# Performance work log

Hardware: AMD Instinct MI355X
Metric: run time of the kernel (lower is better)

The kernel has to match this reference:

```python
import jax, jax.numpy as jnp
import numpy as np

B, N, E = 32, 128, 8192        # graphs, nodes/graph, edges total
IN, ED, H = 64, 32, 128        # node feat, edge feat, hidden
K1, K2, K3 = 64, 32, 16        # ceil(0.5*N) cascade from TopKPooling(ratio=0.5)
EPS = 1e-5


def setup_inputs():
    key = jax.random.key(0)
    ks = jax.random.split(key, 20)
    def rn(i, shape, s=1.0):
        return jax.random.normal(ks[i], shape, dtype=jnp.float32) * s
    x = rn(0, (B * N, IN))
    edge_attr = rn(1, (E, ED))
    epg = E // B  # edges per graph (intra-graph only)
    src = jax.random.randint(ks[2], (B, epg), 0, N)
    dst = jax.random.randint(ks[3], (B, epg), 0, N)
    off = (jnp.arange(B) * N)[:, None]
    edge_index = jnp.stack([(src + off).reshape(-1), (dst + off).reshape(-1)]).astype(jnp.int32)
    batch = jnp.repeat(jnp.arange(B), N).astype(jnp.int32)
    p = {}
    p['nn1_w'] = rn(4, (ED, IN * H), 0.05); p['nn1_b'] = jnp.zeros((IN * H,), jnp.float32)
    p['root1'] = rn(5, (IN, H), 0.1);       p['bias1'] = jnp.zeros((H,), jnp.float32)
    p['nn2_w'] = rn(6, (ED, H * H), 0.05);  p['nn2_b'] = jnp.zeros((H * H,), jnp.float32)
    p['root2'] = rn(7, (H, H), 0.1);        p['bias2'] = jnp.zeros((H,), jnp.float32)
    p['nn3_w'] = rn(8, (ED, H * H), 0.05);  p['nn3_b'] = jnp.zeros((H * H,), jnp.float32)
    p['root3'] = rn(9, (H, H), 0.1);        p['bias3'] = jnp.zeros((H,), jnp.float32)
    for k in ('1', '2', '3'):
        p['gamma' + k] = jnp.ones((H,), jnp.float32)
        p['beta' + k] = jnp.zeros((H,), jnp.float32)
    p['pw1'] = rn(10, (H,), 0.1); p['pw2'] = rn(11, (H,), 0.1); p['pw3'] = rn(12, (H,), 0.1)
    p['lin1_w'] = rn(13, (H, H // 2), 0.1); p['lin1_b'] = jnp.zeros((H // 2,), jnp.float32)
    p['lin2_w'] = rn(14, (H // 2, 1), 0.1); p['lin2_b'] = jnp.zeros((1,), jnp.float32)
    return dict(x=x, edge_index=edge_index, edge_attr=edge_attr, batch=batch, **p)


def _nnconv(x, src, dst, emask, eattr, nn_w, nn_b, root, bias, cin, cout, n_nodes):
    # per-edge weight matrix from edge MLP: [E, cin, cout]
    w = (eattr @ nn_w + nn_b).reshape(-1, cin, cout)
    msg = jnp.einsum('ei,eio->eo', x[src], w) * emask[:, None]  # per-edge matvec
    agg = jnp.zeros((n_nodes, cout), x.dtype).at[dst].add(msg)  # scatter-add aggr
    return agg + x @ root + bias


def _bn(x, gamma, beta):
    mu = x.mean(0)
    var = x.var(0)
    return gamma * (x - mu) * jax.lax.rsqrt(var + EPS) + beta


def _topk_pool(x, src, dst, emask, pw, nb, npg, k):
    # PyG TopKPooling: score = tanh((x.p)/||p||); keep top ceil(ratio*n) per graph
    score = jnp.tanh((x @ pw) / jnp.linalg.norm(pw))            # [nb*npg]
    _, idx = jax.lax.top_k(score.reshape(nb, npg), k)           # [nb, k]
    perm = (idx + (jnp.arange(nb) * npg)[:, None]).reshape(-1)  # global node ids
    x_new = x[perm] * score[perm][:, None]
    mapping = jnp.full((nb * npg,), -1, jnp.int32).at[perm].set(
        jnp.arange(nb * k, dtype=jnp.int32))
    ns, nd = mapping[src], mapping[dst]
    valid = (ns >= 0) & (nd >= 0) & emask   # filter_adj via mask, static shapes
    return x_new, jnp.where(valid, ns, 0), jnp.where(valid, nd, 0), valid


def _forward(x, edge_attr, nn1_w, nn1_b, root1, bias1, gamma1, beta1, pw1,
             nn2_w, nn2_b, root2, bias2, gamma2, beta2, pw2,
             nn3_w, nn3_b, root3, bias3, gamma3, beta3, pw3,
             lin1_w, lin1_b, lin2_w, lin2_b, edge_index):
    src0, dst0 = edge_index[0], edge_index[1]
    m0 = jnp.ones((E,), bool)
    h = _nnconv(x, src0, dst0, m0, edge_attr, nn1_w, nn1_b, root1, bias1, IN, H, B * N)
    h = jax.nn.relu(_bn(h, gamma1, beta1))
    h, s1, d1, m1 = _topk_pool(h, src0, dst0, m0, pw1, B, N, K1)
    h = _nnconv(h, s1, d1, m1, edge_attr, nn2_w, nn2_b, root2, bias2, H, H, B * K1)
    h = jax.nn.relu(_bn(h, gamma2, beta2))
    h, s2, d2, m2 = _topk_pool(h, s1, d1, m1, pw2, B, K1, K2)
    h = _nnconv(h, s2, d2, m2, edge_attr, nn3_w, nn3_b, root3, bias3, H, H, B * K2)
    h = jax.nn.relu(_bn(h, gamma3, beta3))
    h, _, _, _ = _topk_pool(h, s2, d2, m2, pw3, B, K2, K3)
    g = h.reshape(B, K3, H).mean(axis=1)          # global_mean_pool (equal-size graphs)
    g = jax.nn.relu(g @ lin1_w + lin1_b)          # dropout is identity in eval mode
    return jax.nn.sigmoid(g @ lin2_w + lin2_b)    # [B, 1]


def reference(x, edge_index, edge_attr, batch,
              nn1_w, nn1_b, root1, bias1, nn2_w, nn2_b, root2, bias2,
              nn3_w, nn3_b, root3, bias3, gamma1, beta1, gamma2, beta2,
              gamma3, beta3, pw1, pw2, pw3, lin1_w, lin1_b, lin2_w, lin2_b):
    return _forward(x, edge_attr, nn1_w, nn1_b, root1, bias1, gamma1, beta1, pw1,
                    nn2_w, nn2_b, root2, bias2, gamma2, beta2, pw2,
                    nn3_w, nn3_b, root3, bias3, gamma3, beta3, pw3,
                    lin1_w, lin1_b, lin2_w, lin2_b, edge_index)
```

## Files before the change

### kernel.cpp

```cpp
#include <hip/hip_runtime.h>

#define E_TOT 8192
#define NB    32
#define H     128
#define EPG   256
#define NDT   34
#define YD    33
#define YCOLS (YD * H)

#define KH1   2176
#define TROW1 (2 * KH1)
#define KSPLIT1 12

typedef __attribute__((ext_vector_type(8))) short bf16x8;
typedef __attribute__((ext_vector_type(4))) float f32x4;

__device__ __forceinline__ unsigned short bf16_rne(float f) {
    unsigned int u = __float_as_uint(f);
    unsigned int r = (u + 0x7FFFu + ((u >> 16) & 1u)) >> 16;
    return (unsigned short)r;
}
__device__ __forceinline__ float bf16_to_f32(unsigned short h) {
    return __uint_as_float(((unsigned int)h) << 16);
}

__device__ __forceinline__ void gload_lds16(const void* g, void* l) {
    __builtin_amdgcn_global_load_lds(
        (const __attribute__((address_space(1))) unsigned int*)g,
        (__attribute__((address_space(3))) unsigned int*)l, 16, 0, 0);
}

union PrepSMem {
    struct { unsigned short HI[128][72]; unsigned short LO[128][72]; } b1;
    struct { unsigned short HI[128][40]; unsigned short LO[128][40]; } bt;
    struct { float xL[128][64]; float eaL[256][32]; short srcL[256];
             short lists[16][256]; int cnt[16]; } t1;
};

__global__ __launch_bounds__(256)
void prep_all(const float* __restrict__ x, const float* __restrict__ ea,
              const int* __restrict__ esrc, const int* __restrict__ edst,
              const float* __restrict__ nn1w, const float* __restrict__ nn1b,
              const float* __restrict__ root1,
              const float* __restrict__ nn2w, const float* __restrict__ nn2b,
              const float* __restrict__ root2,
              const float* __restrict__ nn3w, const float* __restrict__ nn3b,
              const float* __restrict__ root3,
              unsigned short* __restrict__ Bt1, unsigned short* __restrict__ Bt2,
              unsigned short* __restrict__ Bt3, unsigned short* __restrict__ T1,
              float* __restrict__ stats)
{
    __shared__ PrepSMem sm;
    const int b   = blockIdx.x;
    const int tid = threadIdx.x;

    if (b < 34) {
        if (b == 0)
            for (int i = tid; i < 768; i += 256) stats[i] = 0.f;
        const int d = b;
        const float* __restrict__ W =
            (d < 32) ? (nn1w + (size_t)d * 8192) : ((d == 32) ? nn1b : root1);
        for (int idx = tid; idx < 64 * 128; idx += 256) {
            const int ii = idx >> 7, o = idx & 127;
            const float v = W[ii * 128 + o];
            const unsigned short h = bf16_rne(v);
            sm.b1.HI[o][ii] = h;
            sm.b1.LO[o][ii] = bf16_rne(v - bf16_to_f32(h));
        }
        __syncthreads();
        const int o = tid & 127, half = tid >> 7;
        const uint4* s4 = (const uint4*)(half ? &sm.b1.LO[o][0] : &sm.b1.HI[o][0]);
        uint4* d4 = (uint4*)(Bt1 + (size_t)o * TROW1 + (half ? KH1 : 0) + d * 64);
        #pragma unroll
        for (int q = 0; q < 8; ++q) d4[q] = s4[q];
    } else if (b < 306) {
        const int unit  = b - 34;
        const int stage = unit / 136;
        const int u2    = unit - stage * 136;
        const int d  = u2 >> 2;
        const int i0 = (u2 & 3) * 32;
        const float* __restrict__ W = (stage == 0)
            ? ((d < 32) ? (nn2w + (size_t)d * 16384) : ((d == 32) ? nn2b : root2))
            : ((d < 32) ? (nn3w + (size_t)d * 16384) : ((d == 32) ? nn3b : root3));
        unsigned short* __restrict__ Bt = (stage == 0) ? Bt2 : Bt3;

        for (int idx = tid; idx < 32 * 128; idx += 256) {
            const int ii = idx >> 7, o = idx & 127;
            const float v = W[(size_t)(i0 + ii) * 128 + o];
            const unsigned short h = bf16_rne(v);
            sm.bt.HI[o][ii] = h;
            sm.bt.LO[o][ii] = bf16_rne(v - bf16_to_f32(h));
        }
        __syncthreads();
        const int o = tid & 127, half = tid >> 7;
        unsigned short* dst = Bt + (size_t)(d * 128 + o) * 384;
        const uint4* hs = (const uint4*)&sm.bt.HI[o][0];
        const uint4* ls = (const uint4*)&sm.bt.LO[o][0];
        if (half == 0) {
            uint4* p = (uint4*)(dst + i0);
            p[0] = hs[0]; p[1] = hs[1]; p[2] = hs[2]; p[3] = hs[3];
            uint4* q = (uint4*)(dst + 256 + i0);
            q[0] = ls[0]; q[1] = ls[1]; q[2] = ls[2]; q[3] = ls[3];
        } else {
            uint4* p = (uint4*)(dst + 128 + i0);
            p[0] = hs[0]; p[1] = hs[1]; p[2] = hs[2]; p[3] = hs[3];
        }
    } else {
        const int u    = b - 306;
        const int g    = u >> 3;
        const int base = (u & 7) * 16;
        const int wv   = tid >> 6;
        const int ln   = tid & 63;

        if (tid < 16) sm.t1.cnt[tid] = 0;
        for (int idx = tid; idx < 128 * 64; idx += 256)
            sm.t1.xL[idx >> 6][idx & 63] = x[(size_t)g * 8192 + idx];
        for (int idx = tid; idx < 256 * 32; idx += 256)
            sm.t1.eaL[idx >> 5][idx & 31] = ea[(size_t)g * 8192 + idx];
        __syncthreads();

        {
            const int e = tid;
            sm.t1.srcL[e] = (short)(esrc[g * EPG + e] - g * 128);
            const int r = (edst[g * EPG + e] - g * 128) - base;
            if (r >= 0 && r < 16) {
                const int pos = atomicAdd(&sm.t1.cnt[r], 1);
                sm.t1.lists[r][pos] = (short)e;
            }
        }
        __syncthreads();

        #pragma unroll
        for (int j = 0; j < 4; ++j) {
            const int r = wv * 4 + j;
            const int uu = base + r;
            float acc[33];
            #pragma unroll
            for (int d = 0; d < 33; ++d) acc[d] = 0.f;

            const int n = sm.t1.cnt[r];
            for (int t = 0; t < n; ++t) {
                const int e = sm.t1.lists[r][t];
                const float xv = sm.t1.xL[sm.t1.srcL[e]][ln];
                #pragma unroll
                for (int d = 0; d < 32; ++d) acc[d] += sm.t1.eaL[e][d] * xv;
                acc[32] += xv;
            }

            unsigned short* row = T1 + (size_t)(g * 128 + uu) * TROW1;
            #pragma unroll
            for (int d = 0; d < 33; ++d) {
                const unsigned short hb = bf16_rne(acc[d]);
                row[d * 64 + ln] = hb;
                row[KH1 + d * 64 + ln] = bf16_rne(acc[d] - bf16_to_f32(hb));
            }
            const float xv = sm.t1.xL[uu][ln];
            const unsigned short hb = bf16_rne(xv);
            row[2112 + ln] = hb;
            row[KH1 + 2112 + ln] = bf16_rne(xv - bf16_to_f32(hb));
        }
    }
}

__global__ __launch_bounds__(256)
void hgemm1(const unsigned short* __restrict__ A,
            const unsigned short* __restrict__ Bt,
            const float* __restrict__ bias,
            float* __restrict__ hpart)
{
    __shared__ unsigned short Alds[128 * 32];
    __shared__ unsigned short Blds[128 * 32];

    const int lane = threadIdx.x & 63;
    const int w    = threadIdx.x >> 6;
    const int wm = w >> 1, wn = w & 1;
    const int v0 = blockIdx.x * 128;
    const int c  = blockIdx.y;

    f32x4 acc[4][4];
    #pragma unroll
    for (int i = 0; i < 4; ++i)
        #pragma unroll
        for (int j = 0; j < 4; ++j)
            acc[i][j] = (f32x4)(0.0f);

    const int arow = lane >> 2;
    const int acol = (lane & 3) * 8;
    const int koff = (lane >> 4) * 8;
    const int mrow = lane & 15;

    for (int t = c * 17; t < c * 17 + 17; ++t) {
        const int s  = t / 68;
        const int ko = (t - s * 68) * 32;
        const int aoff = (s == 2 ? KH1 : 0) + ko;
        const int boff = (s == 1 ? KH1 : 0) + ko;

        __syncthreads();
        #pragma unroll
        for (int tt = 0; tt < 2; ++tt) {
            const int cc = w * 2 + tt;
            const int r = cc * 16 + arow;
            gload_lds16(A  + (size_t)(v0 + r) * TROW1 + aoff + acol, &Alds[cc * 512]);
            gload_lds16(Bt + (size_t)r * TROW1 + boff + acol, &Blds[cc * 512]);
        }
        __syncthreads();

        bf16x8 a[4], b[4];
        #pragma unroll
        for (int f = 0; f < 4; ++f) {
            a[f] = *(const bf16x8*)&Alds[(wm * 64 + f * 16 + mrow) * 32 + koff];
            b[f] = *(const bf16x8*)&Blds[(wn * 64 + f * 16 + mrow) * 32 + koff];
        }
        #pragma unroll
        for (int fm = 0; fm < 4; ++fm)
            #pragma unroll
            for (int fn = 0; fn < 4; ++fn)
                acc[fm][fn] = __builtin_amdgcn_mfma_f32_16x16x32_bf16(
                    a[fm], b[fn], acc[fm][fn], 0, 0, 0);
    }

    float* out = hpart + (size_t)c * (4096 * 128);
    const int crow = (lane >> 4) * 4;
    const int ccol = lane & 15;
    #pragma unroll
    for (int fm = 0; fm < 4; ++fm) {
        const int gr = v0 + wm * 64 + fm * 16 + crow;
        #pragma unroll
        for (int fn = 0; fn < 4; ++fn) {
            const int col = wn * 64 + fn * 16 + ccol;
            const float bv = (c == 0) ? bias[col] : 0.f;
            #pragma unroll
            for (int r = 0; r < 4; ++r)
                out[(size_t)(gr + r) * H + col] = acc[fm][fn][r] + bv;
        }
    }
}

__global__ __launch_bounds__(256)
void bn_reduce1(const float* __restrict__ hpart, float* __restrict__ h1,
                float* __restrict__ gsum, float* __restrict__ gsumsq)
{
    const int tid   = threadIdx.x;
    const int col   = tid & 127;
    const int rhalf = tid >> 7;
    float s = 0.f, sq = 0.f;
    for (int r = blockIdx.x * 2 + rhalf; r < 4096; r += gridDim.x * 2) {
        float v = 0.f;
        #pragma unroll
        for (int c = 0; c < KSPLIT1; ++c)
            v += hpart[(size_t)c * (4096 * 128) + (size_t)r * H + col];
        h1[(size_t)r * H + col] = v;
        s += v; sq += v * v;
    }
    __shared__ float sh[256];
    sh[tid] = s;  __syncthreads();
    if (rhalf == 0) s += sh[tid + 128];
    __syncthreads();
    sh[tid] = sq; __syncthreads();
    if (rhalf == 0) {
        sq += sh[tid + 128];
        atomicAdd(&gsum[col], s);
        atomicAdd(&gsumsq[col], sq);
    }
}

template<int K3>
__global__ __launch_bounds__(256)
void ygemm_mfma(const unsigned short* __restrict__ A,
                const unsigned short* __restrict__ Bt,
                float* __restrict__ Y,
                const float* __restrict__ bias,
                float* __restrict__ h)
{
    __shared__ unsigned short Alds[128 * 32];
    __shared__ unsigned short Blds[128 * 32];

    const int lane = threadIdx.x & 63;
    const int w    = threadIdx.x >> 6;
    const int wm = w >> 1, wn = w & 1;
    const int v0 = blockIdx.x * 128;
    const int n0 = blockIdx.y * 128;

    f32x4 acc[4][4];
    #pragma unroll
    for (int i = 0; i < 4; ++i)
        #pragma unroll
        for (int j = 0; j < 4; ++j)
            acc[i][j] = (f32x4)(0.0f);

    const int arow = lane >> 2;
    const int acol = (lane & 3) * 8;
    const int koff = (lane >> 4) * 8;
    const int mrow = lane & 15;

    for (int k0 = 0; k0 < K3; k0 += 32) {
        __syncthreads();
        #pragma unroll
        for (int t = 0; t < 2; ++t) {
            const int c = w * 2 + t;
            const int r = c * 16 + arow;
            gload_lds16(A  + (size_t)(v0 + r) * K3 + k0 + acol, &Alds[c * 512]);
            gload_lds16(Bt + (size_t)(n0 + r) * K3 + k0 + acol, &Blds[c * 512]);
        }
        __syncthreads();

        bf16x8 a[4], b[4];
        #pragma unroll
        for (int f = 0; f < 4; ++f) {
            a[f] = *(const bf16x8*)&Alds[(wm * 64 + f * 16 + mrow) * 32 + koff];
            b[f] = *(const bf16x8*)&Blds[(wn * 64 + f * 16 + mrow) * 32 + koff];
        }
        #pragma unroll
        for (int fm = 0; fm < 4; ++fm)
            #pragma unroll
            for (int fn = 0; fn < 4; ++fn)
                acc[fm][fn] = __builtin_amdgcn_mfma_f32_16x16x32_bf16(
                    a[fm], b[fn], acc[fm][fn], 0, 0, 0);
    }

    const int crow = (lane >> 4) * 4;
    const int ccol = lane & 15;
    const bool is_root = (blockIdx.y == YD);
    #pragma unroll
    for (int fm = 0; fm < 4; ++fm) {
        const int gr = v0 + wm * 64 + fm * 16 + crow;
        #pragma unroll
        for (int fn = 0; fn < 4; ++fn) {
            const int col = wn * 64 + fn * 16 + ccol;
            if (is_root) {
                const float bv = bias[col];
                #pragma unroll
                for (int r = 0; r < 4; ++r)
                    h[(size_t)(gr + r) * H + col] = acc[fm][fn][r] + bv;
            } else {
                const size_t gc = (size_t)blockIdx.y * H + col;
                #pragma unroll
                for (int r = 0; r < 4; ++r)
                    Y[(size_t)(gr + r) * YCOLS + gc] = acc[fm][fn][r];
            }
        }
    }
}

__global__ __launch_bounds__(256)
void contract_edges(const float* __restrict__ Y,
                    const float* __restrict__ ea,
                    const int*   __restrict__ esrc,
                    const int*   __restrict__ edst,
                    float*       __restrict__ agg)
{
    const int grp = threadIdx.x >> 5;
    const int l5  = threadIdx.x & 31;
    const int e   = blockIdx.x * 8 + grp;
    const int s   = esrc[e];
    if (s < 0) return;

    const float* yb  = Y + (size_t)s * YCOLS + l5 * 4;
    const float* ear = ea + (size_t)e * 32;

    float4 acc = *reinterpret_cast<const float4*>(yb + 32 * H);
    #pragma unroll 8
    for (int dd = 0; dd < 32; ++dd) {
        const float c = ear[dd];
        const float4 y = *reinterpret_cast<const float4*>(yb + dd * H);
        acc.x += c * y.x; acc.y += c * y.y; acc.z += c * y.z; acc.w += c * y.w;
    }
    float* out = agg + (size_t)edst[e] * H + l5 * 4;
    atomicAdd(out + 0, acc.x);
    atomicAdd(out + 1, acc.y);
    atomicAdd(out + 2, acc.z);
    atomicAdd(out + 3, acc.w);
}

__global__ __launch_bounds__(256)
void bn_stats(const float* __restrict__ h, int n,
              float* __restrict__ gsum, float* __restrict__ gsumsq)
{
    const int tid   = threadIdx.x;
    const int col   = tid & 127;
    const int rhalf = tid >> 7;
    float s = 0.f, sq = 0.f;
    for (int r = blockIdx.x * 2 + rhalf; r < n; r += gridDim.x * 2) {
        float v = h[(size_t)r * H + col];
        s += v; sq += v * v;
    }
    __shared__ float sh[256];
    sh[tid] = s;  __syncthreads();
    if (rhalf == 0) s += sh[tid + 128];
    __syncthreads();
    sh[tid] = sq; __syncthreads();
    if (rhalf == 0) {
        sq += sh[tid + 128];
        atomicAdd(&gsum[col], s);
        atomicAdd(&gsumsq[col], sq);
    }
}

__global__ __launch_bounds__(256)
void fused_pool(const float* __restrict__ h,
                const float* __restrict__ gsum, const float* __restrict__ gsumsq,
                float n_f,
                const float* __restrict__ gamma, const float* __restrict__ beta,
                const float* __restrict__ pw,
                int npg, int k,
                const int* __restrict__ esrc_in, const int* __restrict__ edst_in,
                int* __restrict__ esrc_out, int* __restrict__ edst_out,
                unsigned short* __restrict__ Aout)
{
    const int g   = blockIdx.x;
    const int tid = threadIdx.x;
    const int wv  = tid >> 6;
    const int ln  = tid & 63;

    __shared__ float muL[128], rsL[128], gmL[128], btL[128], pwL[128];
    __shared__ float scoreL[128], red[128];
    __shared__ int   mapL[128];
    __shared__ float sinv;

    if (tid < 128) {
        const float mu  = gsum[tid] / n_f;
        const float var = gsumsq[tid] / n_f - mu * mu;
        muL[tid] = mu;
        rsL[tid] = rsqrtf(var + 1e-5f);
        gmL[tid] = gamma[tid];
        btL[tid] = beta[tid];
        const float p = pw[tid];
        pwL[tid] = p;
        red[tid] = p * p;
    }
    __syncthreads();
    for (int off = 64; off > 0; off >>= 1) {
        if (tid < off) red[tid] += red[tid + off];
        __syncthreads();
    }
    if (tid == 0) sinv = rsqrtf(red[0]);
    __syncthreads();

    for (int r = wv; r < npg; r += 4) {
        const float* hr = h + (size_t)(g * npg + r) * H;
        float p = 0.f;
        #pragma unroll
        for (int half = 0; half < 2; ++half) {
            const int c = ln + half * 64;
            const float y = fmaxf(gmL[c] * (hr[c] - muL[c]) * rsL[c] + btL[c], 0.f);
            p += y * pwL[c];
        }
        #pragma unroll
        for (int off = 32; off > 0; off >>= 1)
            p += __shfl_down(p, off, 64);
        if (ln == 0) scoreL[r] = tanhf(p * sinv);
    }
    __syncthreads();

    if (tid < npg) {
        const float si = scoreL[tid];
        int cnt = 0;
        for (int j = 0; j < npg; ++j) {
            const float sj = scoreL[j];
            cnt += (sj > si) || (sj == si && j < tid);
        }
        mapL[tid] = (cnt < k) ? cnt : -1;
    }
    __syncthreads();

    for (int r = wv; r < npg; r += 4) {
        const int nr = mapL[r];
        if (nr < 0) continue;
        const float sc = scoreL[r];
        const float* hr = h + (size_t)(g * npg + r) * H;
        unsigned short* arow = Aout + (size_t)(g * k + nr) * 384;
        #pragma unroll
        for (int half = 0; half < 2; ++half) {
            const int c = ln + half * 64;
            const float y = fmaxf(gmL[c] * (hr[c] - muL[c]) * rsL[c] + btL[c], 0.f) * sc;
            const unsigned short hb = bf16_rne(y);
            const unsigned short lb = bf16_rne(y - bf16_to_f32(hb));
            arow[c] = hb; arow[128 + c] = hb; arow[256 + c] = lb;
        }
    }

    {
        const int e = g * EPG + tid;
        const int s = esrc_in[e];
        int ns = -1, nd = -1;
        if (s >= 0) {
            const int ms = mapL[s - g * npg];
            const int md = mapL[edst_in[e] - g * npg];
            if (ms >= 0 && md >= 0) { ns = g * k + ms; nd = g * k + md; }
        }
        esrc_out[e] = ns; edst_out[e] = nd;
    }
}

__global__ __launch_bounds__(256)
void fused_pool_final(const float* __restrict__ h,
                      const float* __restrict__ gsum, const float* __restrict__ gsumsq,
                      float n_f,
                      const float* __restrict__ gamma, const float* __restrict__ beta,
                      const float* __restrict__ pw,
                      const float* __restrict__ lin1_w, const float* __restrict__ lin1_b,
                      const float* __restrict__ lin2_w, const float* __restrict__ lin2_b,
                      float* __restrict__ out)
{
    const int g   = blockIdx.x;
    const int tid = threadIdx.x;
    const int wv  = tid >> 6;
    const int ln  = tid & 63;
    const int npg = 32, k = 16;

    __shared__ float muL[128], rsL[128], gmL[128], btL[128], pwL[128];
    __shared__ float scoreL[32], red[128], gmean[128], h1c[64];
    __shared__ int   mapL[32];
    __shared__ float sinv;

    if (tid < 128) {
        const float mu  = gsum[tid] / n_f;
        const float var = gsumsq[tid] / n_f - mu * mu;
        muL[tid] = mu;
        rsL[tid] = rsqrtf(var + 1e-5f);
        gmL[tid] = gamma[tid];
        btL[tid] = beta[tid];
        const float p = pw[tid];
        pwL[tid] = p;
        red[tid] = p * p;
    }
    __syncthreads();
    for (int off = 64; off > 0; off >>= 1) {
        if (tid < off) red[tid] += red[tid + off];
        __syncthreads();
    }
    if (tid == 0) sinv = rsqrtf(red[0]);
    __syncthreads();

    for (int r = wv; r < npg; r += 4) {
        const float* hr = h + (size_t)(g * npg + r) * H;
        float p = 0.f;
        #pragma unroll
        for (int half = 0; half < 2; ++half) {
            const int c = ln + half * 64;
            const float y = fmaxf(gmL[c] * (hr[c] - muL[c]) * rsL[c] + btL[c], 0.f);
            p += y * pwL[c];
        }
        #pragma unroll
        for (int off = 32; off > 0; off >>= 1)
            p += __shfl_down(p, off, 64);
        if (ln == 0) scoreL[r] = tanhf(p * sinv);
    }
    __syncthreads();

    if (tid < npg) {
        const float si = scoreL[tid];
        int cnt = 0;
        for (int j = 0; j < npg; ++j) {
            const float sj = scoreL[j];
            cnt += (sj > si) || (sj == si && j < tid);
        }
        mapL[tid] = (cnt < k) ? cnt : -1;
    }
    __syncthreads();

    if (tid < 128) {
        float acc = 0.f;
        for (int r = 0; r < npg; ++r) {
            if (mapL[r] < 0) continue;
            const float hv = h[(size_t)(g * npg + r) * H + tid];
            const float y  = fmaxf(gmL[tid] * (hv - muL[tid]) * rsL[tid] + btL[tid], 0.f);
            acc += y * scoreL[r];
        }
        gmean[tid] = acc * (1.0f / 16.0f);
    }
    __syncthreads();

    if (tid < 64) {
        float acc = lin1_b[tid];
        for (int o = 0; o < 128; ++o) acc += gmean[o] * lin1_w[o * 64 + tid];
        h1c[tid] = fmaxf(acc, 0.f);
    }
    __syncthreads();
    if (tid == 0) {
        float z = lin2_b[0];
        for (int j = 0; j < 64; ++j) z += h1c[j] * lin2_w[j];
        out[g] = 1.0f / (1.0f + expf(-z));
    }
}

extern "C" void kernel_launch(void* const* d_in, const int* in_sizes, int n_in,
                              void* d_out, int out_size, void* d_ws, size_t ws_size,
                              hipStream_t stream)
{
    const float* x        = (const float*)d_in[0];
    const int*   ei       = (const int*)  d_in[1];
    const float* eattr    = (const float*)d_in[2];
    const float* nn1_w    = (const float*)d_in[4];
    const float* nn1_b    = (const float*)d_in[5];
    const float* root1    = (const float*)d_in[6];
    const float* bias1    = (const float*)d_in[7];
    const float* nn2_w    = (const float*)d_in[8];
    const float* nn2_b    = (const float*)d_in[9];
    const float* root2    = (const float*)d_in[10];
    const float* bias2    = (const float*)d_in[11];
    const float* nn3_w    = (const float*)d_in[12];
    const float* nn3_b    = (const float*)d_in[13];
    const float* root3    = (const float*)d_in[14];
    const float* bias3    = (const float*)d_in[15];
    const float* gamma1   = (const float*)d_in[16];
    const float* beta1    = (const float*)d_in[17];
    const float* gamma2   = (const float*)d_in[18];
    const float* beta2    = (const float*)d_in[19];
    const float* gamma3   = (const float*)d_in[20];
    const float* beta3    = (const float*)d_in[21];
    const float* pw1      = (const float*)d_in[22];
    const float* pw2      = (const float*)d_in[23];
    const float* pw3      = (const float*)d_in[24];
    const float* lin1_w   = (const float*)d_in[25];
    const float* lin1_b   = (const float*)d_in[26];
    const float* lin2_w   = (const float*)d_in[27];
    const float* lin2_b   = (const float*)d_in[28];

    const int* ei_src = ei;
    const int* ei_dst = ei + E_TOT;

    char* wp = (char*)d_ws;
    auto alloc = [&](size_t bytes) { char* p = wp; wp += (bytes + 255) & ~(size_t)255; return p; };
    float* h1   = (float*)alloc(4096 * 128 * 4);
    float* h2   = (float*)alloc(2048 * 128 * 4);
    float* h3   = (float*)alloc(1024 * 128 * 4);
    int*   src1 = (int*)alloc(E_TOT * 4);
    int*   dst1 = (int*)alloc(E_TOT * 4);
    int*   src2 = (int*)alloc(E_TOT * 4);
    int*   dst2 = (int*)alloc(E_TOT * 4);
    float* stats = (float*)alloc(6 * 128 * 4);
    unsigned short* A2   = (unsigned short*)alloc((size_t)2048 * 384 * 2);
    unsigned short* A3   = (unsigned short*)alloc((size_t)1024 * 384 * 2);
    unsigned short* Bt1n = (unsigned short*)alloc((size_t)128 * TROW1 * 2);
    unsigned short* Bt2  = (unsigned short*)alloc((size_t)4352 * 384 * 2);
    unsigned short* Bt3  = (unsigned short*)alloc((size_t)4352 * 384 * 2);
    unsigned short* T1   = (unsigned short*)alloc((size_t)4096 * TROW1 * 2);
    float* hpart = (float*)alloc((size_t)KSPLIT1 * 4096 * 128 * 4);
    float* Ybuf = (float*)alloc((size_t)2048 * YCOLS * 4);

    prep_all<<<562, 256, 0, stream>>>(x, eattr, ei_src, ei_dst,
                                      nn1_w, nn1_b, root1,
                                      nn2_w, nn2_b, root2,
                                      nn3_w, nn3_b, root3,
                                      Bt1n, Bt2, Bt3, T1, stats);

    hgemm1<<<dim3(32, KSPLIT1), 256, 0, stream>>>(T1, Bt1n, bias1, hpart);
    bn_reduce1<<<256, 256, 0, stream>>>(hpart, h1, stats, stats + 128);
    fused_pool<<<NB, 256, 0, stream>>>(h1, stats, stats + 128, 4096.0f,
                                       gamma1, beta1, pw1, 128, 64,
                                       ei_src, ei_dst, src1, dst1, A2);

    ygemm_mfma<384><<<dim3(16, NDT), 256, 0, stream>>>(A2, Bt2, Ybuf, bias2, h2);
    contract_edges<<<E_TOT / 8, 256, 0, stream>>>(Ybuf, eattr, src1, dst1, h2);
    bn_stats<<<64, 256, 0, stream>>>(h2, 2048, stats + 256, stats + 384);
    fused_pool<<<NB, 256, 0, stream>>>(h2, stats + 256, stats + 384, 2048.0f,
                                       gamma2, beta2, pw2, 64, 32,
                                       src1, dst1, src2, dst2, A3);

    ygemm_mfma<384><<<dim3(8, NDT), 256, 0, stream>>>(A3, Bt3, Ybuf, bias3, h3);
    contract_edges<<<E_TOT / 8, 256, 0, stream>>>(Ybuf, eattr, src2, dst2, h3);
    bn_stats<<<64, 256, 0, stream>>>(h3, 1024, stats + 512, stats + 640);
    fused_pool_final<<<NB, 256, 0, stream>>>(h3, stats + 512, stats + 640, 1024.0f,
                                             gamma3, beta3, pw3,
                                             lin1_w, lin1_b, lin2_w, lin2_b,
                                             (float*)d_out);
}
```

Measured before the change: 291.6 us.

## Reformulate NNConv layers 2 and 3 as edge-contracted T-matrix split-K GEMMs

Layers 2 and 3 previously ran a GEMM producing per-node Y matrices for every edge-feature dimension, followed by a per-edge contraction with float atomics into the output. They now follow the layer-1 scheme: a t_build kernel aggregates edge_attr-weighted source features per destination node into a wide bf16 hi/lo T matrix, and a templated split-K GEMM multiplies it by a reorganized weight layout, with partial sums reduced in bn_reduce. This removes the large Ybuf round trip and the scatter atomics. In exchange it adds the T build pass, a wider K dimension, and a 24-way partial buffer to write and reduce.

After: 309.6 us. +6.2%, slower.

```diff
diff --git a/kernel.cpp b/kernel.cpp
--- a/kernel.cpp
+++ b/kernel.cpp
@@ -4,13 +4,11 @@
 #define NB    32
 #define H     128
 #define EPG   256
-#define NDT   34
-#define YD    33
-#define YCOLS (YD * H)
 
 #define KH1   2176
 #define TROW1 (2 * KH1)
-#define KSPLIT1 12
+#define KH2   4352
+#define TROW2 (2 * KH2)
 
 typedef __attribute__((ext_vector_type(8))) short bf16x8;
 typedef __attribute__((ext_vector_type(4))) float f32x4;
@@ -93,18 +91,10 @@
         }
         __syncthreads();
         const int o = tid & 127, half = tid >> 7;
-        unsigned short* dst = Bt + (size_t)(d * 128 + o) * 384;
-        const uint4* hs = (const uint4*)&sm.bt.HI[o][0];
-        const uint4* ls = (const uint4*)&sm.bt.LO[o][0];
-        if (half == 0) {
-            uint4* p = (uint4*)(dst + i0);
-            p[0] = hs[0]; p[1] = hs[1]; p[2] = hs[2]; p[3] = hs[3];
-            uint4* q = (uint4*)(dst + 256 + i0);
-            q[0] = ls[0]; q[1] = ls[1]; q[2] = ls[2]; q[3] = ls[3];
-        } else {
-            uint4* p = (uint4*)(dst + 128 + i0);
-            p[0] = hs[0]; p[1] = hs[1]; p[2] = hs[2]; p[3] = hs[3];
-        }
+        const uint4* s4 = (const uint4*)(half ? &sm.bt.LO[o][0] : &sm.bt.HI[o][0]);
+        uint4* d4 = (uint4*)(Bt + (size_t)o * TROW2 + (half ? KH2 : 0) + d * 128 + i0);
+        #pragma unroll
+        for (int q = 0; q < 4; ++q) d4[q] = s4[q];
     } else {
         const int u    = b - 306;
         const int g    = u >> 3;
@@ -162,12 +152,89 @@
     }
 }
 
+template<int KROWS>
 __global__ __launch_bounds__(256)
-void hgemm1(const unsigned short* __restrict__ A,
-            const unsigned short* __restrict__ Bt,
-            const float* __restrict__ bias,
-            float* __restrict__ hpart)
+void t_build(const float* __restrict__ x2,
+             const float* __restrict__ ea,
+             const int* __restrict__ esrc, const int* __restrict__ edst,
+             unsigned short* __restrict__ T)
 {
+    const int g    = blockIdx.x;
+    const int base = blockIdx.y * 8;
+    const int tid  = threadIdx.x;
+    const int wv   = tid >> 6;
+    const int ln   = tid & 63;
+
+    __shared__ float xL[KROWS][128];
+    __shared__ float eaL[256][32];
+    __shared__ short srcL[256];
+    __shared__ short lists[8][256];
+    __shared__ int   cnt[8];
+
+    if (tid < 8) cnt[tid] = 0;
+    for (int idx = tid; idx < KROWS * 32; idx += 256)
+        ((float4*)&xL[0][0])[idx] = ((const float4*)(x2 + (size_t)g * KROWS * H))[idx];
+    for (int idx = tid; idx < 256 * 8; idx += 256)
+        ((float4*)&eaL[0][0])[idx] = ((const float4*)(ea + (size_t)g * 8192))[idx];
+    __syncthreads();
+
+    {
+        const int e = tid;
+        srcL[e] = (short)(esrc[g * EPG + e] - g * KROWS);
+        const int r = (edst[g * EPG + e] - g * KROWS) - base;
+        if (r >= 0 && r < 8) {
+            const int pos = atomicAdd(&cnt[r], 1);
+            lists[r][pos] = (short)e;
+        }
+    }
+    __syncthreads();
+
+    #pragma unroll
+    for (int j = 0; j < 2; ++j) {
+        const int r = wv * 2 + j;
+        const int u = base + r;
+        unsigned short* row = T + (size_t)(g * KROWS + u) * TROW2;
+        const int n = cnt[r];
+
+        #pragma unroll
+        for (int half = 0; half < 2; ++half) {
+            const int cc = ln + half * 64;
+            float acc[33];
+            #pragma unroll
+            for (int d = 0; d < 33; ++d) acc[d] = 0.f;
+
+            for (int t = 0; t < n; ++t) {
+                const int e = lists[r][t];
+                const float xv = xL[srcL[e]][cc];
+                #pragma unroll
+                for (int d = 0; d < 32; ++d) acc[d] += eaL[e][d] * xv;
+                acc[32] += xv;
+            }
+
+            #pragma unroll
+            for (int d = 0; d < 33; ++d) {
+                const unsigned short hb = bf16_rne(acc[d]);
+                row[d * 128 + cc] = hb;
+                row[KH2 + d * 128 + cc] = bf16_rne(acc[d] - bf16_to_f32(hb));
+            }
+            const float xv = xL[u][cc];
+            const unsigned short hb = bf16_rne(xv);
+            row[4224 + cc] = hb;
+            row[KH2 + 4224 + cc] = bf16_rne(xv - bf16_to_f32(hb));
+        }
+    }
+}
+
+template<int KHALF>
+__global__ __launch_bounds__(256)
+void hgemm_t(const unsigned short* __restrict__ A,
+             const unsigned short* __restrict__ Bt,
+             const float* __restrict__ bias,
+             float* __restrict__ hpart)
+{
+    constexpr int TROW = 2 * KHALF;
+    constexpr int SEC  = KHALF / 32;
+
     __shared__ unsigned short Alds[128 * 32];
     __shared__ unsigned short Blds[128 * 32];
 
@@ -176,6 +243,7 @@
     const int wm = w >> 1, wn = w & 1;
     const int v0 = blockIdx.x * 128;
     const int c  = blockIdx.y;
+    const int M  = gridDim.x * 128;
 
     f32x4 acc[4][4];
     #pragma unroll
@@ -190,18 +258,18 @@
     const int mrow = lane & 15;
 
     for (int t = c * 17; t < c * 17 + 17; ++t) {
-        const int s  = t / 68;
-        const int ko = (t - s * 68) * 32;
-        const int aoff = (s == 2 ? KH1 : 0) + ko;
-        const int boff = (s == 1 ? KH1 : 0) + ko;
+        const int s  = t / SEC;
+        const int ko = (t - s * SEC) * 32;
+        const int aoff = (s == 2 ? KHALF : 0) + ko;
+        const int boff = (s == 1 ? KHALF : 0) + ko;
 
         __syncthreads();
         #pragma unroll
         for (int tt = 0; tt < 2; ++tt) {
             const int cc = w * 2 + tt;
             const int r = cc * 16 + arow;
-            gload_lds16(A  + (size_t)(v0 + r) * TROW1 + aoff + acol, &Alds[cc * 512]);
-            gload_lds16(Bt + (size_t)r * TROW1 + boff + acol, &Blds[cc * 512]);
+            gload_lds16(A  + (size_t)(v0 + r) * TROW + aoff + acol, &Alds[cc * 512]);
+            gload_lds16(Bt + (size_t)r * TROW + boff + acol, &Blds[cc * 512]);
         }
         __syncthreads();
 
@@ -219,7 +287,7 @@
                     a[fm], b[fn], acc[fm][fn], 0, 0, 0);
     }
 
-    float* out = hpart + (size_t)c * (4096 * 128);
+    float* out = hpart + (size_t)c * M * H;
     const int crow = (lane >> 4) * 4;
     const int ccol = lane & 15;
     #pragma unroll
@@ -236,152 +304,21 @@
     }
 }
 
+template<int NSPLIT>
 __global__ __launch_bounds__(256)
-void bn_reduce1(const float* __restrict__ hpart, float* __restrict__ h1,
-                float* __restrict__ gsum, float* __restrict__ gsumsq)
-{
-    const int tid   = threadIdx.x;
-    const int col   = tid & 127;
-    const int rhalf = tid >> 7;
-    float s = 0.f, sq = 0.f;
-    for (int r = blockIdx.x * 2 + rhalf; r < 4096; r += gridDim.x * 2) {
-        float v = 0.f;
-        #pragma unroll
-        for (int c = 0; c < KSPLIT1; ++c)
-            v += hpart[(size_t)c * (4096 * 128) + (size_t)r * H + col];
-        h1[(size_t)r * H + col] = v;
-        s += v; sq += v * v;
-    }
-    __shared__ float sh[256];
-    sh[tid] = s;  __syncthreads();
-    if (rhalf == 0) s += sh[tid + 128];
-    __syncthreads();
-    sh[tid] = sq; __syncthreads();
-    if (rhalf == 0) {
-        sq += sh[tid + 128];
-        atomicAdd(&gsum[col], s);
-        atomicAdd(&gsumsq[col], sq);
-    }
-}
-
-template<int K3>
-__global__ __launch_bounds__(256)
-void ygemm_mfma(const unsigned short* __restrict__ A,
-                const unsigned short* __restrict__ Bt,
-                float* __restrict__ Y,
-                const float* __restrict__ bias,
-                float* __restrict__ h)
-{
-    __shared__ unsigned short Alds[128 * 32];
-    __shared__ unsigned short Blds[128 * 32];
-
-    const int lane = threadIdx.x & 63;
-    const int w    = threadIdx.x >> 6;
-    const int wm = w >> 1, wn = w & 1;
-    const int v0 = blockIdx.x * 128;
-    const int n0 = blockIdx.y * 128;
-
-    f32x4 acc[4][4];
-    #pragma unroll
-    for (int i = 0; i < 4; ++i)
-        #pragma unroll
-        for (int j = 0; j < 4; ++j)
-            acc[i][j] = (f32x4)(0.0f);
-
-    const int arow = lane >> 2;
-    const int acol = (lane & 3) * 8;
-    const int koff = (lane >> 4) * 8;
-    const int mrow = lane & 15;
-
-    for (int k0 = 0; k0 < K3; k0 += 32) {
-        __syncthreads();
-        #pragma unroll
-        for (int t = 0; t < 2; ++t) {
-            const int c = w * 2 + t;
-            const int r = c * 16 + arow;
-            gload_lds16(A  + (size_t)(v0 + r) * K3 + k0 + acol, &Alds[c * 512]);
-            gload_lds16(Bt + (size_t)(n0 + r) * K3 + k0 + acol, &Blds[c * 512]);
-        }
-        __syncthreads();
-
-        bf16x8 a[4], b[4];
-        #pragma unroll
-        for (int f = 0; f < 4; ++f) {
-            a[f] = *(const bf16x8*)&Alds[(wm * 64 + f * 16 + mrow) * 32 + koff];
-            b[f] = *(const bf16x8*)&Blds[(wn * 64 + f * 16 + mrow) * 32 + koff];
-        }
-        #pragma unroll
-        for (int fm = 0; fm < 4; ++fm)
-            #pragma unroll
-            for (int fn = 0; fn < 4; ++fn)
-                acc[fm][fn] = __builtin_amdgcn_mfma_f32_16x16x32_bf16(
-                    a[fm], b[fn], acc[fm][fn], 0, 0, 0);
-    }
-
-    const int crow = (lane >> 4) * 4;
-    const int ccol = lane & 15;
-    const bool is_root = (blockIdx.y == YD);
-    #pragma unroll
-    for (int fm = 0; fm < 4; ++fm) {
-        const int gr = v0 + wm * 64 + fm * 16 + crow;
-        #pragma unroll
-        for (int fn = 0; fn < 4; ++fn) {
-            const int col = wn * 64 + fn * 16 + ccol;
-            if (is_root) {
-                const float bv = bias[col];
-                #pragma unroll
-                for (int r = 0; r < 4; ++r)
-                    h[(size_t)(gr + r) * H + col] = acc[fm][fn][r] + bv;
-            } else {
-                const size_t gc = (size_t)blockIdx.y * H + col;
-                #pragma unroll
-                for (int r = 0; r < 4; ++r)
-                    Y[(size_t)(gr + r) * YCOLS + gc] = acc[fm][fn][r];
-            }
-        }
-    }
-}
-
-__global__ __launch_bounds__(256)
-void contract_edges(const float* __restrict__ Y,
-                    const float* __restrict__ ea,
-                    const int*   __restrict__ esrc,
-                    const int*   __restrict__ edst,
-                    float*       __restrict__ agg)
-{
-    const int grp = threadIdx.x >> 5;
-    const int l5  = threadIdx.x & 31;
-    const int e   = blockIdx.x * 8 + grp;
-    const int s   = esrc[e];
-    if (s < 0) return;
-
-    const float* yb  = Y + (size_t)s * YCOLS + l5 * 4;
-    const float* ear = ea + (size_t)e * 32;
-
-    float4 acc = *reinterpret_cast<const float4*>(yb + 32 * H);
-    #pragma unroll 8
-    for (int dd = 0; dd < 32; ++dd) {
-        const float c = ear[dd];
-        const float4 y = *reinterpret_cast<const float4*>(yb + dd * H);
-        acc.x += c * y.x; acc.y += c * y.y; acc.z += c * y.z; acc.w += c * y.w;
-    }
-    float* out = agg + (size_t)edst[e] * H + l5 * 4;
-    atomicAdd(out + 0, acc.x);
-    atomicAdd(out + 1, acc.y);
-    atomicAdd(out + 2, acc.z);
-    atomicAdd(out + 3, acc.w);
-}
-
-__global__ __launch_bounds__(256)
-void bn_stats(const float* __restrict__ h, int n,
-              float* __restrict__ gsum, float* __restrict__ gsumsq)
+void bn_reduce(const float* __restrict__ hpart, float* __restrict__ h,
+               float* __restrict__ gsum, float* __restrict__ gsumsq, int n)
 {
     const int tid   = threadIdx.x;
     const int col   = tid & 127;
     const int rhalf = tid >> 7;
     float s = 0.f, sq = 0.f;
     for (int r = blockIdx.x * 2 + rhalf; r < n; r += gridDim.x * 2) {
-        float v = h[(size_t)r * H + col];
+        float v = 0.f;
+        #pragma unroll
+        for (int c = 0; c < NSPLIT; ++c)
+            v += hpart[(size_t)c * n * H + (size_t)r * H + col];
+        h[(size_t)r * H + col] = v;
         s += v; sq += v * v;
     }
     __shared__ float sh[256];
@@ -405,7 +342,7 @@
                 int npg, int k,
                 const int* __restrict__ esrc_in, const int* __restrict__ edst_in,
                 int* __restrict__ esrc_out, int* __restrict__ edst_out,
-                unsigned short* __restrict__ Aout)
+                float* __restrict__ x2out)
 {
     const int g   = blockIdx.x;
     const int tid = threadIdx.x;
@@ -468,14 +405,12 @@
         if (nr < 0) continue;
         const float sc = scoreL[r];
         const float* hr = h + (size_t)(g * npg + r) * H;
-        unsigned short* arow = Aout + (size_t)(g * k + nr) * 384;
+        float* xrow = x2out + (size_t)(g * k + nr) * H;
         #pragma unroll
         for (int half = 0; half < 2; ++half) {
             const int c = ln + half * 64;
-            const float y = fmaxf(gmL[c] * (hr[c] - muL[c]) * rsL[c] + btL[c], 0.f) * sc;
-            const unsigned short hb = bf16_rne(y);
-            const unsigned short lb = bf16_rne(y - bf16_to_f32(hb));
-            arow[c] = hb; arow[128 + c] = hb; arow[256 + c] = lb;
+            const float y = fmaxf(gmL[c] * (hr[c] - muL[c]) * rsL[c] + btL[c], 0.f);
+            xrow[c] = y * sc;
         }
     }
 
@@ -630,37 +565,38 @@
     int*   src2 = (int*)alloc(E_TOT * 4);
     int*   dst2 = (int*)alloc(E_TOT * 4);
     float* stats = (float*)alloc(6 * 128 * 4);
-    unsigned short* A2   = (unsigned short*)alloc((size_t)2048 * 384 * 2);
-    unsigned short* A3   = (unsigned short*)alloc((size_t)1024 * 384 * 2);
+    float* x2   = (float*)alloc((size_t)2048 * 128 * 4);
+    float* x3   = (float*)alloc((size_t)1024 * 128 * 4);
     unsigned short* Bt1n = (unsigned short*)alloc((size_t)128 * TROW1 * 2);
-    unsigned short* Bt2  = (unsigned short*)alloc((size_t)4352 * 384 * 2);
-    unsigned short* Bt3  = (unsigned short*)alloc((size_t)4352 * 384 * 2);
+    unsigned short* Bt2n = (unsigned short*)alloc((size_t)128 * TROW2 * 2);
+    unsigned short* Bt3n = (unsigned short*)alloc((size_t)128 * TROW2 * 2);
     unsigned short* T1   = (unsigned short*)alloc((size_t)4096 * TROW1 * 2);
-    float* hpart = (float*)alloc((size_t)KSPLIT1 * 4096 * 128 * 4);
-    float* Ybuf = (float*)alloc((size_t)2048 * YCOLS * 4);
+    unsigned short* T2   = (unsigned short*)alloc((size_t)2048 * TROW2 * 2);
+    unsigned short* T3   = (unsigned short*)alloc((size_t)1024 * TROW2 * 2);
+    float* hpart = (float*)alloc((size_t)24 * 2048 * 128 * 4);
 
     prep_all<<<562, 256, 0, stream>>>(x, eattr, ei_src, ei_dst,
                                       nn1_w, nn1_b, root1,
                                       nn2_w, nn2_b, root2,
                                       nn3_w, nn3_b, root3,
-                                      Bt1n, Bt2, Bt3, T1, stats);
-
-    hgemm1<<<dim3(32, KSPLIT1), 256, 0, stream>>>(T1, Bt1n, bias1, hpart);
-    bn_reduce1<<<256, 256, 0, stream>>>(hpart, h1, stats, stats + 128);
+                                      Bt1n, Bt2n, Bt3n, T1, stats);
+
+    hgemm_t<KH1><<<dim3(32, 12), 256, 0, stream>>>(T1, Bt1n, bias1, hpart);
+    bn_reduce<12><<<256, 256, 0, stream>>>(hpart, h1, stats, stats + 128, 4096);
     fused_pool<<<NB, 256, 0, stream>>>(h1, stats, stats + 128, 4096.0f,
                                        gamma1, beta1, pw1, 128, 64,
-                                       ei_src, ei_dst, src1, dst1, A2);
-
-    ygemm_mfma<384><<<dim3(16, NDT), 256, 0, stream>>>(A2, Bt2, Ybuf, bias2, h2);
-    contract_edges<<<E_TOT / 8, 256, 0, stream>>>(Ybuf, eattr, src1, dst1, h2);
-    bn_stats<<<64, 256, 0, stream>>>(h2, 2048, stats + 256, stats + 384);
+                                       ei_src, ei_dst, src1, dst1, x2);
+
+    t_build<64><<<dim3(NB, 8), 256, 0, stream>>>(x2, eattr, src1, dst1, T2);
+    hgemm_t<KH2><<<dim3(16, 24), 256, 0, stream>>>(T2, Bt2n, bias2, hpart);
+    bn_reduce<24><<<256, 256, 0, stream>>>(hpart, h2, stats + 256, stats + 384, 2048);
     fused_pool<<<NB, 256, 0, stream>>>(h2, stats + 256, stats + 384, 2048.0f,
                                        gamma2, beta2, pw2, 64, 32,
-                                       src1, dst1, src2, dst2, A3);
-
-    ygemm_mfma<384><<<dim3(8, NDT), 256, 0, stream>>>(A3, Bt3, Ybuf, bias3, h3);
-    contract_edges<<<E_TOT / 8, 256, 0, stream>>>(Ybuf, eattr, src2, dst2, h3);
-    bn_stats<<<64, 256, 0, stream>>>(h3, 1024, stats + 512, stats + 640);
+                                       src1, dst1, src2, dst2, x3);
+
+    t_build<32><<<dim3(NB, 4), 256, 0, stream>>>(x3, eattr, src2, dst2, T3);
+    hgemm_t<KH2><<<dim3(8, 24), 256, 0, stream>>>(T3, Bt3n, bias3, hpart);
+    bn_reduce<24><<<256, 256, 0, stream>>>(hpart, h3, stats + 512, stats + 640, 1024);
     fused_pool_final<<<NB, 256, 0, stream>>>(h3, stats + 512, stats + 640, 1024.0f,
                                              gamma3, beta3, pw3,
                                              lin1_w, lin1_b, lin2_w, lin2_b,
```

## Fuse post-GEMM stages into persistent kernels with global atomic barriers

Applied to the files above, without the earlier changes.

Merges bn_reduce1 with the first pool, and contract_edges, bn_stats and pool for the later stages, into three persistent 256-block kernels. The stages inside each kernel are separated by atomic-counter grid barriers instead of kernel boundaries. The goal is to remove several kernel launches and the gaps between them. In exchange, all 256 blocks must be co-resident or the spin-waits deadlock, and contract_edges now loops over edges with fewer blocks than before.

Result: slower. 371.3 us (+27.3%).

```diff
diff --git a/kernel.cpp b/kernel.cpp
--- a/kernel.cpp
+++ b/kernel.cpp
@@ -11,6 +11,7 @@
 #define KH1   2176
 #define TROW1 (2 * KH1)
 #define KSPLIT1 12
+#define KH2   4352
 
 typedef __attribute__((ext_vector_type(8))) short bf16x8;
 typedef __attribute__((ext_vector_type(4))) float f32x4;
@@ -28,6 +29,17 @@
     __builtin_amdgcn_global_load_lds(
         (const __attribute__((address_space(1))) unsigned int*)g,
         (__attribute__((address_space(3))) unsigned int*)l, 16, 0, 0);
+}
+
+__device__ __forceinline__ void sig_done(int* cnt) {
+    __syncthreads();
+    if (threadIdx.x == 0) { __threadfence(); atomicAdd(cnt, 1); }
+}
+__device__ __forceinline__ void wait_done(int* cnt, int target) {
+    if (threadIdx.x == 0)
+        while (atomicAdd(cnt, 0) < target) __builtin_amdgcn_s_sleep(8);
+    __syncthreads();
+    __threadfence();
 }
 
 union PrepSMem {
@@ -48,15 +60,17 @@
               const float* __restrict__ root3,
               unsigned short* __restrict__ Bt1, unsigned short* __restrict__ Bt2,
               unsigned short* __restrict__ Bt3, unsigned short* __restrict__ T1,
-              float* __restrict__ stats)
+              float* __restrict__ stats, int* __restrict__ cnts)
 {
     __shared__ PrepSMem sm;
     const int b   = blockIdx.x;
     const int tid = threadIdx.x;
 
     if (b < 34) {
-        if (b == 0)
+        if (b == 0) {
             for (int i = tid; i < 768; i += 256) stats[i] = 0.f;
+            if (tid < 8) cnts[tid] = 0;
+        }
         const int d = b;
         const float* __restrict__ W =
             (d < 32) ? (nn1w + (size_t)d * 8192) : ((d == 32) ? nn1b : root1);
@@ -233,34 +247,6 @@
             for (int r = 0; r < 4; ++r)
                 out[(size_t)(gr + r) * H + col] = acc[fm][fn][r] + bv;
         }
-    }
-}
-
-__global__ __launch_bounds__(256)
-void bn_reduce1(const float* __restrict__ hpart, float* __restrict__ h1,
-                float* __restrict__ gsum, float* __restrict__ gsumsq)
-{
-    const int tid   = threadIdx.x;
-    const int col   = tid & 127;
-    const int rhalf = tid >> 7;
-    float s = 0.f, sq = 0.f;
-    for (int r = blockIdx.x * 2 + rhalf; r < 4096; r += gridDim.x * 2) {
-        float v = 0.f;
-        #pragma unroll
-        for (int c = 0; c < KSPLIT1; ++c)
-            v += hpart[(size_t)c * (4096 * 128) + (size_t)r * H + col];
-        h1[(size_t)r * H + col] = v;
-        s += v; sq += v * v;
-    }
-    __shared__ float sh[256];
-    sh[tid] = s;  __syncthreads();
-    if (rhalf == 0) s += sh[tid + 128];
-    __syncthreads();
-    sh[tid] = sq; __syncthreads();
-    if (rhalf == 0) {
-        sq += sh[tid + 128];
-        atomicAdd(&gsum[col], s);
-        atomicAdd(&gsumsq[col], sq);
     }
 }
 
@@ -342,49 +328,49 @@
     }
 }
 
-__global__ __launch_bounds__(256)
-void contract_edges(const float* __restrict__ Y,
-                    const float* __restrict__ ea,
-                    const int*   __restrict__ esrc,
-                    const int*   __restrict__ edst,
-                    float*       __restrict__ agg)
+__device__ void contract_body(int nb, int bid,
+                              const float* __restrict__ Y,
+                              const float* __restrict__ ea,
+                              const int*   __restrict__ esrc,
+                              const int*   __restrict__ edst,
+                              float*       __restrict__ agg)
 {
     const int grp = threadIdx.x >> 5;
     const int l5  = threadIdx.x & 31;
-    const int e   = blockIdx.x * 8 + grp;
-    const int s   = esrc[e];
-    if (s < 0) return;
-
-    const float* yb  = Y + (size_t)s * YCOLS + l5 * 4;
-    const float* ear = ea + (size_t)e * 32;
-
-    float4 acc = *reinterpret_cast<const float4*>(yb + 32 * H);
-    #pragma unroll 8
-    for (int dd = 0; dd < 32; ++dd) {
-        const float c = ear[dd];
-        const float4 y = *reinterpret_cast<const float4*>(yb + dd * H);
-        acc.x += c * y.x; acc.y += c * y.y; acc.z += c * y.z; acc.w += c * y.w;
-    }
-    float* out = agg + (size_t)edst[e] * H + l5 * 4;
-    atomicAdd(out + 0, acc.x);
-    atomicAdd(out + 1, acc.y);
-    atomicAdd(out + 2, acc.z);
-    atomicAdd(out + 3, acc.w);
-}
-
-__global__ __launch_bounds__(256)
-void bn_stats(const float* __restrict__ h, int n,
-              float* __restrict__ gsum, float* __restrict__ gsumsq)
-{
+    for (int b = bid; b < E_TOT / 8; b += nb) {
+        const int e = b * 8 + grp;
+        const int s = esrc[e];
+        if (s >= 0) {
+            const float* yb  = Y + (size_t)s * YCOLS + l5 * 4;
+            const float* ear = ea + (size_t)e * 32;
+            float4 acc = *reinterpret_cast<const float4*>(yb + 32 * H);
+            #pragma unroll 8
+            for (int dd = 0; dd < 32; ++dd) {
+                const float c = ear[dd];
+                const float4 y = *reinterpret_cast<const float4*>(yb + dd * H);
+                acc.x += c * y.x; acc.y += c * y.y; acc.z += c * y.z; acc.w += c * y.w;
+            }
+            float* out = agg + (size_t)edst[e] * H + l5 * 4;
+            atomicAdd(out + 0, acc.x);
+            atomicAdd(out + 1, acc.y);
+            atomicAdd(out + 2, acc.z);
+            atomicAdd(out + 3, acc.w);
+        }
+    }
+}
+
+__device__ void bn_stats_body(int nb, int bid, const float* __restrict__ h, int n,
+                              float* __restrict__ gsum, float* __restrict__ gsumsq)
+{
+    __shared__ float sh[256];
     const int tid   = threadIdx.x;
     const int col   = tid & 127;
     const int rhalf = tid >> 7;
     float s = 0.f, sq = 0.f;
-    for (int r = blockIdx.x * 2 + rhalf; r < n; r += gridDim.x * 2) {
+    for (int r = bid * 2 + rhalf; r < n; r += nb * 2) {
         float v = h[(size_t)r * H + col];
         s += v; sq += v * v;
     }
-    __shared__ float sh[256];
     sh[tid] = s;  __syncthreads();
     if (rhalf == 0) s += sh[tid + 128];
     __syncthreads();
@@ -394,20 +380,48 @@
         atomicAdd(&gsum[col], s);
         atomicAdd(&gsumsq[col], sq);
     }
-}
-
-__global__ __launch_bounds__(256)
-void fused_pool(const float* __restrict__ h,
-                const float* __restrict__ gsum, const float* __restrict__ gsumsq,
-                float n_f,
-                const float* __restrict__ gamma, const float* __restrict__ beta,
-                const float* __restrict__ pw,
-                int npg, int k,
-                const int* __restrict__ esrc_in, const int* __restrict__ edst_in,
-                int* __restrict__ esrc_out, int* __restrict__ edst_out,
-                unsigned short* __restrict__ Aout)
-{
-    const int g   = blockIdx.x;
+    __syncthreads();
+}
+
+__device__ void bn_reduce_body(int nb, int bid, const float* __restrict__ hpart,
+                               float* __restrict__ h, float* __restrict__ gsum,
+                               float* __restrict__ gsumsq, int n)
+{
+    __shared__ float sh[256];
+    const int tid   = threadIdx.x;
+    const int col   = tid & 127;
+    const int rhalf = tid >> 7;
+    float s = 0.f, sq = 0.f;
+    for (int r = bid * 2 + rhalf; r < n; r += nb * 2) {
+        float v = 0.f;
+        #pragma unroll
+        for (int c = 0; c < KSPLIT1; ++c)
+            v += hpart[(size_t)c * n * H + (size_t)r * H + col];
+        h[(size_t)r * H + col] = v;
+        s += v; sq += v * v;
+    }
+    sh[tid] = s;  __syncthreads();
+    if (rhalf == 0) s += sh[tid + 128];
+    __syncthreads();
+    sh[tid] = sq; __syncthreads();
+    if (rhalf == 0) {
+        sq += sh[tid + 128];
+        atomicAdd(&gsum[col], s);
+        atomicAdd(&gsumsq[col], sq);
+    }
+    __syncthreads();
+}
+
+__device__ void pool_body(int g, const float* __restrict__ h,
+                          const float* __restrict__ gsum, const float* __restrict__ gsumsq,
+                          float n_f,
+                          const float* __restrict__ gamma, const float* __restrict__ beta,
+                          const float* __restrict__ pw,
+                          int npg, int k,
+                          const int* __restrict__ esrc_in, const int* __restrict__ edst_in,
+                          int* __restrict__ esrc_out, int* __restrict__ edst_out,
+                          unsigned short* __restrict__ Aout)
+{
     const int tid = threadIdx.x;
     const int wv  = tid >> 6;
     const int ln  = tid & 63;
@@ -492,17 +506,15 @@
     }
 }
 
-__global__ __launch_bounds__(256)
-void fused_pool_final(const float* __restrict__ h,
-                      const float* __restrict__ gsum, const float* __restrict__ gsumsq,
-                      float n_f,
-                      const float* __restrict__ gamma, const float* __restrict__ beta,
-                      const float* __restrict__ pw,
-                      const float* __restrict__ lin1_w, const float* __restrict__ lin1_b,
-                      const float* __restrict__ lin2_w, const float* __restrict__ lin2_b,
-                      float* __restrict__ out)
-{
-    const int g   = blockIdx.x;
+__device__ void pool_final_body(int g, const float* __restrict__ h,
+                                const float* __restrict__ gsum, const float* __restrict__ gsumsq,
+                                float n_f,
+                                const float* __restrict__ gamma, const float* __restrict__ beta,
+                                const float* __restrict__ pw,
+                                const float* __restrict__ lin1_w, const float* __restrict__ lin1_b,
+                                const float* __restrict__ lin2_w, const float* __restrict__ lin2_b,
+                                float* __restrict__ out)
+{
     const int tid = threadIdx.x;
     const int wv  = tid >> 6;
     const int ln  = tid & 63;
@@ -581,6 +593,67 @@
         float z = lin2_b[0];
         for (int j = 0; j < 64; ++j) z += h1c[j] * lin2_w[j];
         out[g] = 1.0f / (1.0f + expf(-z));
+    }
+}
+
+__global__ __launch_bounds__(256)
+void mega_s1(const float* __restrict__ hpart, float* __restrict__ h1,
+             float* __restrict__ stats,
+             const float* __restrict__ gamma, const float* __restrict__ beta,
+             const float* __restrict__ pw,
+             const int* __restrict__ esrc, const int* __restrict__ edst,
+             int* __restrict__ src1, int* __restrict__ dst1,
+             unsigned short* __restrict__ A2, int* __restrict__ cnt)
+{
+    bn_reduce_body(256, blockIdx.x, hpart, h1, stats, stats + 128, 4096);
+    sig_done(cnt);
+    if (blockIdx.x < NB) {
+        wait_done(cnt, 256);
+        pool_body(blockIdx.x, h1, stats, stats + 128, 4096.0f, gamma, beta, pw,
+                  128, 64, esrc, edst, src1, dst1, A2);
+    }
+}
+
+__global__ __launch_bounds__(256)
+void mega_s2(const float* __restrict__ Y, const float* __restrict__ ea,
+             const int* __restrict__ esrc_in, const int* __restrict__ edst_in,
+             float* __restrict__ h2, float* __restrict__ stats,
+             const float* __restrict__ gamma, const float* __restrict__ beta,
+             const float* __restrict__ pw,
+             int* __restrict__ esrc_out, int* __restrict__ edst_out,
+             unsigned short* __restrict__ A3, int* __restrict__ cnt)
+{
+    contract_body(256, blockIdx.x, Y, ea, esrc_in, edst_in, h2);
+    sig_done(cnt);
+    wait_done(cnt, 256);
+    bn_stats_body(256, blockIdx.x, h2, 2048, stats, stats + 128);
+    sig_done(cnt + 1);
+    if (blockIdx.x < NB) {
+        wait_done(cnt + 1, 256);
+        pool_body(blockIdx.x, h2, stats, stats + 128, 2048.0f, gamma, beta, pw,
+                  64, 32, esrc_in, edst_in, esrc_out, edst_out, A3);
+    }
+}
+
+__global__ __launch_bounds__(256)
+void mega_s3(const float* __restrict__ Y, const float* __restrict__ ea,
+             const int* __restrict__ esrc_in, const int* __restrict__ edst_in,
+             float* __restrict__ h3, float* __restrict__ stats,
+             const float* __restrict__ gamma, const float* __restrict__ beta,
+             const float* __restrict__ pw,
+             const float* __restrict__ lin1_w, const float* __restrict__ lin1_b,
+             const float* __restrict__ lin2_w, const float* __restrict__ lin2_b,
+             float* __restrict__ out, int* __restrict__ cnt)
+{
+    contract_body(256, blockIdx.x, Y, ea, esrc_in, edst_in, h3);
+    sig_done(cnt);
+    wait_done(cnt, 256);
+    bn_stats_body(256, blockIdx.x, h3, 1024, stats, stats + 128);
+    sig_done(cnt + 1);
+    if (blockIdx.x < NB) {
+        wait_done(cnt + 1, 256);
+        pool_final_body(blockIdx.x, h3, stats, stats + 128, 1024.0f, gamma, beta, pw,
+                        lin1_w, lin1_b, lin2_w, lin2_b, out);
     }
 }
 
@@ -630,6 +703,7 @@
     int*   src2 = (int*)alloc(E_TOT * 4);
     int*   dst2 = (int*)alloc(E_TOT * 4);
     float* stats = (float*)alloc(6 * 128 * 4);
+    int*   cnts  = (int*)alloc(8 * 4);
     unsigned short* A2   = (unsigned short*)alloc((size_t)2048 * 384 * 2);
     unsigned short* A3   = (unsigned short*)alloc((size_t)1024 * 384 * 2);
     unsigned short* Bt1n = (unsigned short*)alloc((size_t)128 * TROW1 * 2);
@@ -637,32 +711,25 @@
     unsigned short* Bt3  = (unsigned short*)alloc((size_t)4352 * 384 * 2);
     unsigned short* T1   = (unsigned short*)alloc((size_t)4096 * TROW1 * 2);
     float* hpart = (float*)alloc((size_t)KSPLIT1 * 4096 * 128 * 4);
-    float* Ybuf = (float*)alloc((size_t)2048 * YCOLS * 4);
+    float* Ybuf  = (float*)alloc((size_t)2048 * YCOLS * 4);
 
     prep_all<<<562, 256, 0, stream>>>(x, eattr, ei_src, ei_dst,
                                       nn1_w, nn1_b, root1,
                                       nn2_w, nn2_b, root2,
                                       nn3_w, nn3_b, root3,
-                                      Bt1n, Bt2, Bt3, T1, stats);
+                                      Bt1n, Bt2, Bt3, T1, stats, cnts);
 
     hgemm1<<<dim3(32, KSPLIT1), 256, 0, stream>>>(T1, Bt1n, bias1, hpart);
-    bn_reduce1<<<256, 256, 0, stream>>>(hpart, h1, stats, stats + 128);
-    fused_pool<<<NB, 256, 0, stream>>>(h1, stats, stats + 128, 4096.0f,
-                                       gamma1, beta1, pw1, 128, 64,
-                                       ei_src, ei_dst, src1, dst1, A2);
+    mega_s1<<<256, 256, 0, stream>>>(hpart, h1, stats, gamma1, beta1, pw1,
+                                     ei_src, ei_dst, src1, dst1, A2, cnts);
 
     ygemm_mfma<384><<<dim3(16, NDT), 256, 0, stream>>>(A2, Bt2, Ybuf, bias2, h2);
-    contract_edges<<<E_TOT / 8, 256, 0, stream>>>(Ybuf, eattr, src1, dst1, h2);
-    bn_stats<<<64, 256, 0, stream>>>(h2, 2048, stats + 256, stats + 384);
-    fused_pool<<<NB, 256, 0, stream>>>(h2, stats + 256, stats + 384, 2048.0f,
-                                       gamma2, beta2, pw2, 64, 32,
-                                       src1, dst1, src2, dst2, A3);
+    mega_s2<<<256, 256, 0, stream>>>(Ybuf, eattr, src1, dst1, h2, stats + 256,
+                                     gamma2, beta2, pw2, src2, dst2, A3, cnts + 2);
 
     ygemm_mfma<384><<<dim3(8, NDT), 256, 0, stream>>>(A3, Bt3, Ybuf, bias3, h3);
-    contract_edges<<<E_TOT / 8, 256, 0, stream>>>(Ybuf, eattr, src2, dst2, h3);
-    bn_stats<<<64, 256, 0, stream>>>(h3, 1024, stats + 512, stats + 640);
-    fused_pool_final<<<NB, 256, 0, stream>>>(h3, stats + 512, stats + 640, 1024.0f,
-                                             gamma3, beta3, pw3,
-                                             lin1_w, lin1_b, lin2_w, lin2_b,
-                                             (float*)d_out);
-}
+    mega_s3<<<256, 256, 0, stream>>>(Ybuf, eattr, src2, dst2, h3, stats + 512,
+                                     gamma3, beta3, pw3,
+                                     lin1_w, lin1_b, lin2_w, lin2_b,
+                                     (float*)d_out, cnts + 4);
+}
```
